# Kernel optimization log

Measured on AMD Instinct MI355X. Metric: run time of the kernel, lower is better.

## Reference

```python
import jax, jax.numpy as jnp
import numpy as np

EPS = 1e-5
H = W = 14  # spatial grid, N = H*W = 196


def layernorm(x, g, b):
    m = x.mean(-1, keepdims=True)
    v = ((x - m) ** 2).mean(-1, keepdims=True)
    return (x - m) * jax.lax.rsqrt(v + EPS) * g + b


def fem_step(x, s):
    # x: [B, C, H, W]; blockwise instance-norm -> sigmoid gate -> 0.5*x + 0.5*attn*x
    B, C, h, w = x.shape
    nbh = -(-h // s)
    nbw = -(-w // s)
    idh = np.arange(h) // s
    idw = np.arange(w) // s
    bid_np = (idh[:, None] * nbw + idw[None, :]).reshape(-1)  # [h*w]
    cnt = jnp.asarray(np.bincount(bid_np, minlength=nbh * nbw).astype(np.float32))
    bid = jnp.asarray(bid_np)
    xt = x.reshape(B, C, h * w).transpose(2, 0, 1)  # [HW, B, C]
    s1 = jax.ops.segment_sum(xt, bid, num_segments=nbh * nbw)      # [nblk, B, C]
    s2 = jax.ops.segment_sum(xt * xt, bid, num_segments=nbh * nbw)
    mean = s1 / cnt[:, None, None]
    var = s2 / cnt[:, None, None] - mean * mean  # biased var, as F.instance_norm
    attn = jax.nn.sigmoid((xt - mean[bid]) * jax.lax.rsqrt(var[bid] + EPS))
    out = 0.5 * xt * (1.0 + attn)  # 0.5*x + 0.5*attn*x
    return out.transpose(1, 2, 0).reshape(B, C, h, w)


def fem(x):
    # p=[2,1,0] -> block sizes H//4=3, H//2=7, H//1=14
    for s in (H // 4, H // 2, H):
        x = fem_step(x, s)
    return x


def setup_inputs() -> dict:
    key = jax.random.key(0)
    ks = jax.random.split(key, 4)
    B, N, C = 64, H * W, 1024
    hid = 4 * C
    return {
        "x": jax.random.normal(ks[0], (B, N, C), jnp.float32),
        "ln1_g": jnp.ones((C,), jnp.float32),
        "ln1_b": jnp.zeros((C,), jnp.float32),
        "cw": jax.random.normal(ks[1], (H, W // 2 + 1, C, 2), jnp.float32) * 0.02,
        "ln2_g": jnp.ones((C,), jnp.float32),
        "ln2_b": jnp.zeros((C,), jnp.float32),
        "fc1_w": jax.random.normal(ks[2], (C, hid), jnp.float32) * 0.02,
        "fc1_b": jnp.zeros((hid,), jnp.float32),
        "fc2_w": jax.random.normal(ks[3], (hid, C), jnp.float32) * 0.02,
        "fc2_b": jnp.zeros((C,), jnp.float32),
    }


def reference(x, ln1_g, ln1_b, cw, ln2_g, ln2_b, fc1_w, fc1_b, fc2_w, fc2_b):
    B, N, C = x.shape
    # FFT global filter
    y = layernorm(x, ln1_g, ln1_b)
    yf = jnp.fft.rfft2(y.reshape(B, H, W, C), axes=(1, 2), norm="ortho")
    yf = yf * (cw[..., 0] + 1j * cw[..., 1])
    y = jnp.fft.irfft2(yf, s=(H, W), axes=(1, 2), norm="ortho").reshape(B, N, C)
    # MLP
    y = layernorm(y, ln2_g, ln2_b)
    y = jax.nn.gelu(y @ fc1_w + fc1_b, approximate=False) @ fc2_w + fc2_b
    # FEM on [B, C, H, W]
    y = fem(y.transpose(0, 2, 1).reshape(B, C, H, W))
    y = y.reshape(B, C, N).transpose(0, 2, 1)
    return x + y
```

## Files before the change

kernel.cpp:

```cpp
#include <hip/hip_runtime.h>

constexpr int CB = 64;
constexpr int CHH = 14, CWW = 14;
constexpr int CN = 196;
constexpr int CC = 1024;
constexpr int CROWS = CB * CN;
constexpr int CKW = 8;

constexpr float C14[14] = {
  1.0f, 0.9009688679024191f, 0.6234898018587336f, 0.2225209339563144f,
  -0.2225209339563144f, -0.6234898018587336f, -0.9009688679024191f, -1.0f,
  -0.9009688679024191f, -0.6234898018587336f, -0.2225209339563144f,
  0.2225209339563144f, 0.6234898018587336f, 0.9009688679024191f };
constexpr float S14[14] = {
  0.0f, 0.4338837391175581f, 0.7818314824680298f, 0.9749279121818236f,
  0.9749279121818236f, 0.7818314824680298f, 0.4338837391175581f, 0.0f,
  -0.4338837391175581f, -0.7818314824680298f, -0.9749279121818236f,
  -0.9749279121818236f, -0.7818314824680298f, -0.4338837391175581f };

typedef __attribute__((ext_vector_type(8))) short bf16x8;
typedef __attribute__((ext_vector_type(4))) float f32x4;

__device__ __forceinline__ unsigned short f2bf(float f) {
  unsigned u = __builtin_bit_cast(unsigned, f);
  u += 0x7FFFu + ((u >> 16) & 1u);
  return (unsigned short)(u >> 16);
}
__device__ __forceinline__ float bf2f(unsigned short h) {
  return __builtin_bit_cast(float, (unsigned)h << 16);
}

__device__ __forceinline__ void gload_lds16(const void* g, void* l) {
  __builtin_amdgcn_global_load_lds(
      (const __attribute__((address_space(1))) void*)g,
      (__attribute__((address_space(3))) void*)l, 16, 0, 0);
}

#define WAITV(N)  asm volatile("s_waitcnt vmcnt(" #N ")" ::: "memory")
#define SBAR()    asm volatile("s_barrier" ::: "memory")
#define WAITLGKM0() asm volatile("s_waitcnt lgkmcnt(0)" ::: "memory")

template<int OUTBF>
__global__ __launch_bounds__(256)
void ln_kernel(const float* __restrict__ in, const float* __restrict__ gam,
               const float* __restrict__ bet, float* __restrict__ outf,
               unsigned short* __restrict__ outb)
{
  const int row = blockIdx.x;
  const int t = threadIdx.x;
  const float4 v = *(const float4*)(in + (size_t)row * CC + t * 4);
  float s  = v.x + v.y + v.z + v.w;
  float s2 = v.x*v.x + v.y*v.y + v.z*v.z + v.w*v.w;
  #pragma unroll
  for (int o = 32; o > 0; o >>= 1) { s += __shfl_down(s, o); s2 += __shfl_down(s2, o); }
  __shared__ float red[8];
  const int wid = t >> 6, lane = t & 63;
  if (lane == 0) { red[wid] = s; red[4 + wid] = s2; }
  __syncthreads();
  s  = red[0] + red[1] + red[2] + red[3];
  s2 = red[4] + red[5] + red[6] + red[7];
  const float mean = s * (1.0f / CC);
  const float var  = s2 * (1.0f / CC) - mean * mean;
  const float r = rsqrtf(var + 1e-5f);
  const float4 g4 = *(const float4*)(gam + t * 4);
  const float4 b4 = *(const float4*)(bet + t * 4);
  const float o0 = (v.x - mean) * r * g4.x + b4.x;
  const float o1 = (v.y - mean) * r * g4.y + b4.y;
  const float o2 = (v.z - mean) * r * g4.z + b4.z;
  const float o3 = (v.w - mean) * r * g4.w + b4.w;
  if (OUTBF) {
    ushort4 p; p.x = f2bf(o0); p.y = f2bf(o1); p.z = f2bf(o2); p.w = f2bf(o3);
    *(ushort4*)(outb + (size_t)row * CC + t * 4) = p;
  } else {
    *(float4*)(outf + (size_t)row * CC + t * 4) = make_float4(o0, o1, o2, o3);
  }
}

__global__ __launch_bounds__(256)
void fft_w_fwd(const float* __restrict__ y, float* __restrict__ Ar, float* __restrict__ Ai)
{
  const int t = threadIdx.x;
  const int bid = blockIdx.x;
  const int cc = bid & 3;
  const int tmp = bid >> 2;
  const int h = tmp % 14;
  const int b = tmp / 14;
  const int c = cc * 256 + t;
  const size_t base = ((size_t)b * CN + (size_t)h * CWW) * CC + c;
  float v[14];
  #pragma unroll
  for (int w = 0; w < 14; w++) v[w] = y[base + (size_t)w * CC];
  const size_t obase = (((size_t)b * CHH + h) * CKW) * CC + c;
  #pragma unroll
  for (int kw = 0; kw < 8; kw++) {
    float sr = 0.f, si = 0.f;
    #pragma unroll
    for (int w = 0; w < 14; w++) {
      const int m = (w * kw) % 14;
      sr += v[w] * C14[m];
      si -= v[w] * S14[m];
    }
    Ar[obase + (size_t)kw * CC] = sr;
    Ai[obase + (size_t)kw * CC] = si;
  }
}

__global__ __launch_bounds__(256)
void fft_h_filt(const float* __restrict__ Ar, const float* __restrict__ Ai,
                const float* __restrict__ cw, float* __restrict__ Br, float* __restrict__ Bi)
{
  const int t = threadIdx.x;
  const int bid = blockIdx.x;
  const int cc = bid & 3;
  const int tmp = bid >> 2;
  const int kw = tmp & 7;
  const int b = tmp >> 3;
  const int c = cc * 256 + t;
  const size_t base = (((size_t)b * CHH) * CKW + kw) * CC + c;
  float ar[14], ai[14];
  #pragma unroll
  for (int h = 0; h < 14; h++) {
    ar[h] = Ar[base + (size_t)h * (CKW * CC)];
    ai[h] = Ai[base + (size_t)h * (CKW * CC)];
  }
  float fr[14], fi[14];
  #pragma unroll
  for (int kh = 0; kh < 14; kh++) {
    float yr = 0.f, yi = 0.f;
    #pragma unroll
    for (int h = 0; h < 14; h++) {
      const int m = (h * kh) % 14;
      yr += ar[h] * C14[m] + ai[h] * S14[m];
      yi += ai[h] * C14[m] - ar[h] * S14[m];
    }
    const size_t widx = (((size_t)kh * CKW + kw) * CC + c) * 2;
    const float wr = cw[widx], wi = cw[widx + 1];
    fr[kh] = yr * wr - yi * wi;
    fi[kh] = yr * wi + yi * wr;
  }
  #pragma unroll
  for (int h = 0; h < 14; h++) {
    float sr = 0.f, si = 0.f;
    #pragma unroll
    for (int kh = 0; kh < 14; kh++) {
      const int m = (h * kh) % 14;
      sr += fr[kh] * C14[m] - fi[kh] * S14[m];
      si += fr[kh] * S14[m] + fi[kh] * C14[m];
    }
    Br[base + (size_t)h * (CKW * CC)] = sr;
    Bi[base + (size_t)h * (CKW * CC)] = si;
  }
}

__global__ __launch_bounds__(256)
void fft_w_inv(const float* __restrict__ Br, const float* __restrict__ Bi, float* __restrict__ y2)
{
  const int t = threadIdx.x;
  const int bid = blockIdx.x;
  const int cc = bid & 3;
  const int tmp = bid >> 2;
  const int h = tmp % 14;
  const int b = tmp / 14;
  const int c = cc * 256 + t;
  const size_t ibase = (((size_t)b * CHH + h) * CKW) * CC + c;
  float br[8], bi[8];
  #pragma unroll
  for (int k = 0; k < 8; k++) {
    br[k] = Br[ibase + (size_t)k * CC];
    bi[k] = Bi[ibase + (size_t)k * CC];
  }
  const size_t obase = ((size_t)b * CN + (size_t)h * CWW) * CC + c;
  #pragma unroll
  for (int w = 0; w < 14; w++) {
    float s = br[0] + ((w & 1) ? -br[7] : br[7]);
    #pragma unroll
    for (int k = 1; k < 7; k++) {
      const int m = (w * k) % 14;
      s += 2.0f * (br[k] * C14[m] - bi[k] * S14[m]);
    }
    y2[obase + (size_t)w * CC] = s * (1.0f / 196.0f);
  }
}

__global__ __launch_bounds__(256)
void transpose_f32_bf16(const float* __restrict__ in, unsigned short* __restrict__ out,
                        int R, int Ccols)
{
  __shared__ float tile[32][33];
  const int tx = threadIdx.x & 31;
  const int ty = threadIdx.x >> 5;
  const int cb = blockIdx.x * 32;
  const int rb = blockIdx.y * 32;
  #pragma unroll
  for (int i = 0; i < 32; i += 8)
    tile[ty + i][tx] = in[(size_t)(rb + ty + i) * Ccols + cb + tx];
  __syncthreads();
  #pragma unroll
  for (int i = 0; i < 32; i += 8)
    out[(size_t)(cb + ty + i) * R + rb + tx] = f2bf(tile[tx][ty + i]);
}

#define STAGE(REG, TILE_, BUF_) do {                                          \
  char* _tb = sm + ((BUF_) << 16) + (((REG) < 2) ? 0 : 32768);                \
  const unsigned short* _g = (((REG) < 2) ? A : BT);                          \
  const int _gb = (((REG) < 2) ? brow : bcol);                                \
  int _r0, _r1;                                                               \
  if ((REG) == 0)      { _r0 = vA;       _r1 = 128 + vA; }                    \
  else if ((REG) == 1) { _r0 = 64 + vA;  _r1 = 192 + vA; }                    \
  else if ((REG) == 2) { _r0 = ((vA>>5)<<6) + (vA&31);      _r1 = _r0 + 128; }\
  else                 { _r0 = ((vA>>5)<<6) + 32 + (vA&31); _r1 = _r0 + 128; }\
  const int _gc = (TILE_) * 64 + cl;                                          \
  gload_lds16(_g + (size_t)(_gb + _r0) * K + _gc, _tb + _r0 * 128 + dcol16);  \
  gload_lds16(_g + (size_t)(_gb + _r1) * K + _gc, _tb + _r1 * 128 + dcol16);  \
} while (0)

#define PHASE(TT, BUF, PH) do {                                               \
  const char* At_ = sm + ((BUF) << 16);                                       \
  const char* Bt_ = At_ + 32768;                                              \
  if (((PH) & 1) == 0) {                                                      \
    const int mh_ = (PH) >> 1;                                                \
    _Pragma("unroll")                                                         \
    for (int mf = 0; mf < 4; ++mf) {                                          \
      const int row = wm * 128 + mh_ * 64 + mf * 16 + lrow;                   \
      const int sw = (row & 7) << 4;                                          \
      af[mf][0] = *(const bf16x8*)(At_ + row * 128 + ((0  | dq) ^ sw));       \
      af[mf][1] = *(const bf16x8*)(At_ + row * 128 + ((64 | dq) ^ sw));       \
    }                                                                         \
  }                                                                           \
  {                                                                           \
    const int nh_ = (PH) & 1;                                                 \
    _Pragma("unroll")                                                         \
    for (int nf = 0; nf < 2; ++nf) {                                          \
      const int row = wn * 64 + (nh_ * 2 + nf) * 16 + lrow;                   \
      const int sw = (row & 7) << 4;                                          \
      bfr[nf][0] = *(const bf16x8*)(Bt_ + row * 128 + ((0  | dq) ^ sw));      \
      bfr[nf][1] = *(const bf16x8*)(Bt_ + row * 128 + ((64 | dq) ^ sw));      \
    }                                                                         \
  }                                                                           \
  if ((PH) == 0)      { if ((TT) + 1 >= 2 && (TT) + 1 < NT) STAGE(1, (TT)+1, (BUF)^1); } \
  else if ((PH) == 1) { if ((TT) + 1 >= 2 && (TT) + 1 < NT) STAGE(3, (TT)+1, (BUF)^1); } \
  else if ((PH) == 2) { if ((TT) + 2 < NT) STAGE(0, (TT)+2, (BUF)); }         \
  else                { if ((TT) + 2 < NT) STAGE(2, (TT)+2, (BUF)); }         \
  if ((PH) == 0)      { if ((TT) >= NT - 2) { WAITV(0); } else { WAITV(10); } } \
  else if ((PH) == 1) { if ((TT) < NT - 2) { WAITV(8); } }                    \
  else if ((PH) == 2) { if ((TT) < NT - 2) { WAITV(12); } }                   \
  SBAR();                                                                     \
  WAITLGKM0();                                                                \
  __builtin_amdgcn_s_setprio(1);                                              \
  {                                                                           \
    const int mh_ = (PH) >> 1, nh_ = (PH) & 1;                                \
    _Pragma("unroll")                                                         \
    for (int ks = 0; ks < 2; ++ks)                                            \
      _Pragma("unroll")                                                       \
      for (int mf = 0; mf < 4; ++mf)                                          \
        _Pragma("unroll")                                                     \
        for (int nf = 0; nf < 2; ++nf)                                        \
          acc[mh_ * 4 + mf][nh_ * 2 + nf] = __builtin_amdgcn_mfma_f32_16x16x32_bf16( \
              af[mf][ks], bfr[nf][ks], acc[mh_ * 4 + mf][nh_ * 2 + nf], 0, 0, 0); \
  }                                                                           \
  __builtin_amdgcn_s_setprio(0);                                              \
  SBAR();                                                                     \
} while (0)

#define KTILE(TT, BUF) do {                                                   \
  PHASE(TT, BUF, 0); PHASE(TT, BUF, 1); PHASE(TT, BUF, 2); PHASE(TT, BUF, 3); \
} while (0)

template<int DO_GELU>
__global__ __launch_bounds__(512, 2)
void gemm256(const unsigned short* __restrict__ A, const unsigned short* __restrict__ BT,
             const float* __restrict__ bias, unsigned short* __restrict__ C,
             int M, int N, int K)
{
  extern __shared__ __align__(16) char sm[];
  const int t = threadIdx.x;
  const int wid = t >> 6, lane = t & 63;
  const int wm = wid >> 2, wn = wid & 3;
  const int lrow = lane & 15, qk = lane >> 4;
  const int dq = qk << 4;

  const int nbx = N >> 8, nby = M >> 8;
  const int nwg = nbx * nby;
  const int orig = blockIdx.x;
  const int q8 = nwg >> 3, r8 = nwg & 7, xcd = orig & 7, lid = orig >> 3;
  const int wg = (xcd < r8 ? xcd * (q8 + 1) : r8 * (q8 + 1) + (xcd - r8) * q8) + lid;
  const int gw = 4 * nby;
  const int gid = wg / gw, rem = wg % gw;
  const int bx = gid * 4 + (rem & 3);
  const int by = rem >> 2;
  const int brow = by << 8, bcol = bx << 8;
  const int NT = K >> 6;

  const int vA = t >> 3;
  const int cl = ((t ^ (t >> 3)) & 7) << 3;
  const int dcol16 = (t & 7) << 4;

  f32x4 acc[8][4] = {};
  bf16x8 af[4][2], bfr[2][2];

  STAGE(0, 0, 0); STAGE(2, 0, 0); STAGE(1, 0, 0); STAGE(3, 0, 0);
  STAGE(0, 1, 1); STAGE(2, 1, 1); STAGE(1, 1, 1); STAGE(3, 1, 1);
  WAITV(8);
  SBAR();

  for (int T = 0; T < NT; T += 2) {
    KTILE(T, 0);
    KTILE(T + 1, 1);
  }

  #pragma unroll
  for (int mf = 0; mf < 8; ++mf) {
    #pragma unroll
    for (int nf = 0; nf < 4; ++nf) {
      const int ccol = bcol + wn * 64 + nf * 16 + lrow;
      const float bb = bias[ccol];
      #pragma unroll
      for (int j = 0; j < 4; ++j) {
        const int r = brow + wm * 128 + mf * 16 + qk * 4 + j;
        float v = acc[mf][nf][j] + bb;
        if (DO_GELU) v = 0.5f * v * (1.0f + erff(v * 0.70710678118654752f));
        C[(size_t)r * N + ccol] = f2bf(v);
      }
    }
  }
}

__device__ __forceinline__ void fem_block(unsigned short* col, int t,
                                          int h0, int nh, int w0, int nw)
{
  float s = 0.f, s2 = 0.f;
  for (int ih = 0; ih < nh; ih++)
    for (int iw = 0; iw < nw; iw++) {
      const float v = bf2f(col[((h0 + ih) * 14 + w0 + iw) * 128 + t]);
      s += v; s2 += v * v;
    }
  const float inv = 1.0f / (float)(nh * nw);
  const float m = s * inv;
  const float var = s2 * inv - m * m;
  const float r = rsqrtf(var + 1e-5f);
  for (int ih = 0; ih < nh; ih++)
    for (int iw = 0; iw < nw; iw++) {
      const int idx = ((h0 + ih) * 14 + w0 + iw) * 128 + t;
      const float v = bf2f(col[idx]);
      const float a = 1.0f / (1.0f + __expf(-(v - m) * r));
      col[idx] = f2bf(0.5f * v * (1.0f + a));
    }
}

__global__ __launch_bounds__(128)
void fem_kernel(const unsigned short* __restrict__ z, const float* __restrict__ x,
                float* __restrict__ out)
{
  __shared__ unsigned short buf[CN * 128];
  const int t = threadIdx.x;
  const int b = blockIdx.x >> 3;
  const int cc = blockIdx.x & 7;
  const int c = cc * 128 + t;
  const size_t base = (size_t)b * CN * CC + c;
  #pragma unroll 4
  for (int n = 0; n < CN; n++) buf[n * 128 + t] = z[base + (size_t)n * CC];
  const int st3[5] = {0, 3, 6, 9, 12};
  const int ln3[5] = {3, 3, 3, 3, 2};
  for (int i = 0; i < 5; i++)
    for (int j = 0; j < 5; j++)
      fem_block(buf, t, st3[i], ln3[i], st3[j], ln3[j]);
  for (int i = 0; i < 2; i++)
    for (int j = 0; j < 2; j++)
      fem_block(buf, t, i * 7, 7, j * 7, 7);
  fem_block(buf, t, 0, 14, 0, 14);
  #pragma unroll 4
  for (int n = 0; n < CN; n++)
    out[base + (size_t)n * CC] = x[base + (size_t)n * CC] + bf2f(buf[n * 128 + t]);
}

extern "C" void kernel_launch(void* const* d_in, const int* in_sizes, int n_in,
                              void* d_out, int out_size, void* d_ws, size_t ws_size,
                              hipStream_t stream) {
  const float* x     = (const float*)d_in[0];
  const float* ln1_g = (const float*)d_in[1];
  const float* ln1_b = (const float*)d_in[2];
  const float* cw    = (const float*)d_in[3];
  const float* ln2_g = (const float*)d_in[4];
  const float* ln2_b = (const float*)d_in[5];
  const float* fc1_w = (const float*)d_in[6];
  const float* fc1_b = (const float*)d_in[7];
  const float* fc2_w = (const float*)d_in[8];
  const float* fc2_b = (const float*)d_in[9];
  float* out = (float*)d_out;
  char* ws = (char*)d_ws;

  const size_t SZ_A = (size_t)CB * CHH * CKW * CC * 4;
  float* Ar = (float*)(ws);
  float* Ai = (float*)(ws + SZ_A);
  float* Br = (float*)(ws + 2 * SZ_A);
  float* Bi = (float*)(ws + 3 * SZ_A);
  unsigned short* A1   = (unsigned short*)(ws);
  unsigned short* W1T  = (unsigned short*)(ws + SZ_A);
  unsigned short* W2T  = (unsigned short*)(ws + SZ_A + (size_t)4096 * 1024 * 2);
  unsigned short* Hmid = (unsigned short*)(ws + 2 * SZ_A);
  unsigned short* Z    = (unsigned short*)(ws);

  static bool attr_done = false;
  if (!attr_done) {
    hipFuncSetAttribute((const void*)gemm256<1>,
                        hipFuncAttributeMaxDynamicSharedMemorySize, 131072);
    hipFuncSetAttribute((const void*)gemm256<0>,
                        hipFuncAttributeMaxDynamicSharedMemorySize, 131072);
    attr_done = true;
  }

  ln_kernel<0><<<CROWS, 256, 0, stream>>>(x, ln1_g, ln1_b, out, nullptr);
  fft_w_fwd<<<CB * CHH * 4, 256, 0, stream>>>(out, Ar, Ai);
  fft_h_filt<<<CB * CKW * 4, 256, 0, stream>>>(Ar, Ai, cw, Br, Bi);
  fft_w_inv<<<CB * CHH * 4, 256, 0, stream>>>(Br, Bi, out);
  ln_kernel<1><<<CROWS, 256, 0, stream>>>(out, ln2_g, ln2_b, nullptr, A1);
  transpose_f32_bf16<<<dim3(4096 / 32, 1024 / 32), 256, 0, stream>>>(fc1_w, W1T, 1024, 4096);
  transpose_f32_bf16<<<dim3(1024 / 32, 4096 / 32), 256, 0, stream>>>(fc2_w, W2T, 4096, 1024);
  gemm256<1><<<dim3(784), 512, 131072, stream>>>(A1, W1T, fc1_b, Hmid, CROWS, 4096, 1024);
  gemm256<0><<<dim3(196), 512, 131072, stream>>>(Hmid, W2T, fc2_b, Z, CROWS, 1024, 4096);
  fem_kernel<<<CB * 8, 128, 0, stream>>>(Z, x, out);
}
```

Before: 516.2 us.

## Restructure GEMM LDS pipeline into double-buffered one-tile-ahead prefetch with fewer barriers

Replaces the dynamic 128 KB LDS layout with four static A/B tile buffers and swaps them between even and odd K-tiles. Each phase now stages one quarter of the next tile into the alternate buffer, instead of prefetching two tiles ahead into split halves. The trailing barrier in each phase is dropped and a scheduling barrier is added before the MFMA block. The aim is to cut synchronisation overhead and simplify the wait counts. In exchange, global-load latency is hidden only one tile ahead, which risks stalls, and LDS reuse may race without the removed barrier.

```diff
diff --git a/kernel.cpp b/kernel.cpp
--- a/kernel.cpp
+++ b/kernel.cpp
@@ -200,8 +200,7 @@
     out[(size_t)(cb + ty + i) * R + rb + tx] = f2bf(tile[tx][ty + i]);
 }
 
-#define STAGE(REG, TILE_, BUF_) do {                                          \
-  char* _tb = sm + ((BUF_) << 16) + (((REG) < 2) ? 0 : 32768);                \
+#define STAGE(REG, TILE_, DST) do {                                           \
   const unsigned short* _g = (((REG) < 2) ? A : BT);                          \
   const int _gb = (((REG) < 2) ? brow : bcol);                                \
   int _r0, _r1;                                                               \
@@ -210,21 +209,19 @@
   else if ((REG) == 2) { _r0 = ((vA>>5)<<6) + (vA&31);      _r1 = _r0 + 128; }\
   else                 { _r0 = ((vA>>5)<<6) + 32 + (vA&31); _r1 = _r0 + 128; }\
   const int _gc = (TILE_) * 64 + cl;                                          \
-  gload_lds16(_g + (size_t)(_gb + _r0) * K + _gc, _tb + _r0 * 128 + dcol16);  \
-  gload_lds16(_g + (size_t)(_gb + _r1) * K + _gc, _tb + _r1 * 128 + dcol16);  \
+  gload_lds16(_g + (size_t)(_gb + _r0) * K + _gc, (DST) + _r0 * 128 + dcol16);\
+  gload_lds16(_g + (size_t)(_gb + _r1) * K + _gc, (DST) + _r1 * 128 + dcol16);\
 } while (0)
 
-#define PHASE(TT, BUF, PH) do {                                               \
-  const char* At_ = sm + ((BUF) << 16);                                       \
-  const char* Bt_ = At_ + 32768;                                              \
+#define PHASE(TT, CA, CB, NA, NB, PH) do {                                    \
   if (((PH) & 1) == 0) {                                                      \
     const int mh_ = (PH) >> 1;                                                \
     _Pragma("unroll")                                                         \
     for (int mf = 0; mf < 4; ++mf) {                                          \
       const int row = wm * 128 + mh_ * 64 + mf * 16 + lrow;                   \
       const int sw = (row & 7) << 4;                                          \
-      af[mf][0] = *(const bf16x8*)(At_ + row * 128 + ((0  | dq) ^ sw));       \
-      af[mf][1] = *(const bf16x8*)(At_ + row * 128 + ((64 | dq) ^ sw));       \
+      af[mf][0] = *(const bf16x8*)((CA) + row * 128 + ((0  | dq) ^ sw));      \
+      af[mf][1] = *(const bf16x8*)((CA) + row * 128 + ((64 | dq) ^ sw));      \
     }                                                                         \
   }                                                                           \
   {                                                                           \
@@ -233,19 +230,22 @@
     for (int nf = 0; nf < 2; ++nf) {                                          \
       const int row = wn * 64 + (nh_ * 2 + nf) * 16 + lrow;                   \
       const int sw = (row & 7) << 4;                                          \
-      bfr[nf][0] = *(const bf16x8*)(Bt_ + row * 128 + ((0  | dq) ^ sw));      \
-      bfr[nf][1] = *(const bf16x8*)(Bt_ + row * 128 + ((64 | dq) ^ sw));      \
+      bfr[nf][0] = *(const bf16x8*)((CB) + row * 128 + ((0  | dq) ^ sw));     \
+      bfr[nf][1] = *(const bf16x8*)((CB) + row * 128 + ((64 | dq) ^ sw));     \
     }                                                                         \
   }                                                                           \
-  if ((PH) == 0)      { if ((TT) + 1 >= 2 && (TT) + 1 < NT) STAGE(1, (TT)+1, (BUF)^1); } \
-  else if ((PH) == 1) { if ((TT) + 1 >= 2 && (TT) + 1 < NT) STAGE(3, (TT)+1, (BUF)^1); } \
-  else if ((PH) == 2) { if ((TT) + 2 < NT) STAGE(0, (TT)+2, (BUF)); }         \
-  else                { if ((TT) + 2 < NT) STAGE(2, (TT)+2, (BUF)); }         \
-  if ((PH) == 0)      { if ((TT) >= NT - 2) { WAITV(0); } else { WAITV(10); } } \
-  else if ((PH) == 1) { if ((TT) < NT - 2) { WAITV(8); } }                    \
-  else if ((PH) == 2) { if ((TT) < NT - 2) { WAITV(12); } }                   \
+  if ((TT) + 1 < NT) {                                                        \
+    if ((PH) == 0)      STAGE(0, (TT)+1, NA);                                 \
+    else if ((PH) == 1) STAGE(2, (TT)+1, NB);                                 \
+    else if ((PH) == 2) STAGE(3, (TT)+1, NB);                                 \
+    else                STAGE(1, (TT)+1, NA);                                 \
+  }                                                                           \
+  if ((PH) == 0)      { if ((TT) == NT - 1) { WAITV(0); } else { WAITV(6); } }\
+  else if ((PH) == 1) { WAITV(6); }                                           \
+  else if ((PH) == 2) { WAITV(6); }                                           \
   SBAR();                                                                     \
   WAITLGKM0();                                                                \
+  __builtin_amdgcn_sched_barrier(0);                                          \
   __builtin_amdgcn_s_setprio(1);                                              \
   {                                                                           \
     const int mh_ = (PH) >> 1, nh_ = (PH) & 1;                                \
@@ -259,11 +259,11 @@
               af[mf][ks], bfr[nf][ks], acc[mh_ * 4 + mf][nh_ * 2 + nf], 0, 0, 0); \
   }                                                                           \
   __builtin_amdgcn_s_setprio(0);                                              \
-  SBAR();                                                                     \
 } while (0)
 
-#define KTILE(TT, BUF) do {                                                   \
-  PHASE(TT, BUF, 0); PHASE(TT, BUF, 1); PHASE(TT, BUF, 2); PHASE(TT, BUF, 3); \
+#define KTILE(TT, CA, CB, NA, NB) do {                                        \
+  PHASE(TT, CA, CB, NA, NB, 0); PHASE(TT, CA, CB, NA, NB, 1);                 \
+  PHASE(TT, CA, CB, NA, NB, 2); PHASE(TT, CA, CB, NA, NB, 3);                 \
 } while (0)
 
 template<int DO_GELU>
@@ -272,7 +272,13 @@
              const float* __restrict__ bias, unsigned short* __restrict__ C,
              int M, int N, int K)
 {
-  extern __shared__ __align__(16) char sm[];
+  __shared__ __align__(16) short A0s[256 * 64];
+  __shared__ __align__(16) short A1s[256 * 64];
+  __shared__ __align__(16) short B0s[256 * 64];
+  __shared__ __align__(16) short B1s[256 * 64];
+  char* a0 = (char*)A0s; char* a1 = (char*)A1s;
+  char* b0 = (char*)B0s; char* b1 = (char*)B1s;
+
   const int t = threadIdx.x;
   const int wid = t >> 6, lane = t & 63;
   const int wm = wid >> 2, wn = wid & 3;
@@ -298,14 +304,13 @@
   f32x4 acc[8][4] = {};
   bf16x8 af[4][2], bfr[2][2];
 
-  STAGE(0, 0, 0); STAGE(2, 0, 0); STAGE(1, 0, 0); STAGE(3, 0, 0);
-  STAGE(0, 1, 1); STAGE(2, 1, 1); STAGE(1, 1, 1); STAGE(3, 1, 1);
-  WAITV(8);
+  STAGE(0, 0, a0); STAGE(2, 0, b0); STAGE(3, 0, b0); STAGE(1, 0, a0);
+  WAITV(0);
   SBAR();
 
   for (int T = 0; T < NT; T += 2) {
-    KTILE(T, 0);
-    KTILE(T + 1, 1);
+    KTILE(T,     a0, b0, a1, b1);
+    KTILE(T + 1, a1, b1, a0, b0);
   }
 
   #pragma unroll
@@ -400,15 +405,6 @@
   unsigned short* Hmid = (unsigned short*)(ws + 2 * SZ_A);
   unsigned short* Z    = (unsigned short*)(ws);
 
-  static bool attr_done = false;
-  if (!attr_done) {
-    hipFuncSetAttribute((const void*)gemm256<1>,
-                        hipFuncAttributeMaxDynamicSharedMemorySize, 131072);
-    hipFuncSetAttribute((const void*)gemm256<0>,
-                        hipFuncAttributeMaxDynamicSharedMemorySize, 131072);
-    attr_done = true;
-  }
-
   ln_kernel<0><<<CROWS, 256, 0, stream>>>(x, ln1_g, ln1_b, out, nullptr);
   fft_w_fwd<<<CB * CHH * 4, 256, 0, stream>>>(out, Ar, Ai);
   fft_h_filt<<<CB * CKW * 4, 256, 0, stream>>>(Ar, Ai, cw, Br, Bi);
@@ -416,7 +412,7 @@
   ln_kernel<1><<<CROWS, 256, 0, stream>>>(out, ln2_g, ln2_b, nullptr, A1);
   transpose_f32_bf16<<<dim3(4096 / 32, 1024 / 32), 256, 0, stream>>>(fc1_w, W1T, 1024, 4096);
   transpose_f32_bf16<<<dim3(1024 / 32, 4096 / 32), 256, 0, stream>>>(fc2_w, W2T, 4096, 1024);
-  gemm256<1><<<dim3(784), 512, 131072, stream>>>(A1, W1T, fc1_b, Hmid, CROWS, 4096, 1024);
-  gemm256<0><<<dim3(196), 512, 131072, stream>>>(Hmid, W2T, fc2_b, Z, CROWS, 1024, 4096);
+  gemm256<1><<<dim3(784), 512, 0, stream>>>(A1, W1T, fc1_b, Hmid, CROWS, 4096, 1024);
+  gemm256<0><<<dim3(196), 512, 0, stream>>>(Hmid, W2T, fc2_b, Z, CROWS, 1024, 4096);
   fem_kernel<<<CB * 8, 128, 0, stream>>>(Z, x, out);
 }
```

Result: faster. 493.4 us (-4.4%).
